# Optimization experiments

Hardware: AMD Instinct MI355X
Metric: run time of the kernel (lower is better)

Reference implementation:

```python
import jax, jax.numpy as jnp
import numpy as np

DELTA = 0.0  # default `delta` arg of forward


def _features(voxels, clust_ids, num_clusters):
    # voxels: [N,3] float, clust_ids: [N] int in [0, C)
    n = voxels.shape[0]
    seg = lambda x: jax.ops.segment_sum(x, clust_ids, num_segments=num_clusters)
    counts = seg(jnp.ones((n,), voxels.dtype))                     # [C] cluster sizes
    safe_cnt = jnp.maximum(counts, 1.0)
    center = seg(voxels) / safe_cnt[:, None]                       # [C,3] per-cluster mean
    xc = voxels - center[clust_ids]                                # [N,3] centered voxels
    cov = seg(xc[:, :, None] * xc[:, None, :])                     # [C,3,3] = x^T x per cluster
    w, v = jnp.linalg.eigh(cov)                                    # eigvals ascending (== torch.eig + argsort)
    w2 = w[:, 2]
    dirwt = jnp.where(w2 == 0, 0.0, 1.0 - w[:, 1] / jnp.where(w2 == 0, 1.0, w2))
    wd = w + DELTA
    denom = jnp.where(wd[:, 2] == 0, 1.0, wd[:, 2])
    wn = wd / denom[:, None]                                       # w normalized by largest
    eye = jnp.eye(3, dtype=voxels.dtype)
    B = (1.0 - DELTA) * jnp.einsum('cij,cj,ckj->cik', v, wn, v) + DELTA * eye  # [C,3,3]
    v0 = v[:, :, 2]                                                # [C,3] principal axis
    x0 = jnp.sum(xc * v0[clust_ids], axis=-1)                      # [N] projection on v0
    xp0 = xc - x0[:, None] * v0[clust_ids]                         # [N,3] residual
    np0 = jnp.linalg.norm(xp0, axis=1)                             # [N]
    sc = seg(x0 * np0)                                             # [C] sign score
    v0 = jnp.where((sc < 0)[:, None], -v0, v0) * dirwt[:, None]
    # len(c) < 2 branch: center = the voxel itself (mean handles it), B = delta*I, v0 = 0
    small = counts < 2.0
    B = jnp.where(small[:, None, None], DELTA * eye, B)
    v0 = jnp.where(small[:, None], 0.0, v0)
    return jnp.concatenate([center, B.reshape(num_clusters, 9), v0, counts[:, None]], axis=1)  # [C,16]


def setup_inputs() -> dict:
    key = jax.random.key(0)
    k1, k2 = jax.random.split(key)
    n, c = 4000000, 4096
    data = jax.random.normal(k1, (n, 5), dtype=jnp.float32)
    clust_ids = jax.random.randint(k2, (n,), 0, c)
    return {"data": data, "clust_ids": clust_ids, "num_clusters": c}


def reference(data, clust_ids, num_clusters):
    voxels = data[:, :3].astype(jnp.float32)
    return _features(voxels, clust_ids, num_clusters)
```

## Files before the change

kernel.cpp:

```cpp
#include <hip/hip_runtime.h>
#include <math.h>

#define NC 4096
#define OVCAP 131072
#define CAP1 8520

__device__ __forceinline__ int xcd_id() {
    return (int)__builtin_amdgcn_s_getreg(20 | (0 << 6) | ((4 - 1) << 11));
}

__device__ __forceinline__ void solve_cluster(const float mom[10], float* o,
                                              float4* pcv, float4* pvv) {
    float cntf = mom[0];
    double dn  = (double)cntf;
    double inv = 1.0 / fmax(dn, 1.0);
    double cx = mom[1] * inv, cy = mom[2] * inv, cz = mom[3] * inv;

    double a00 = (double)mom[4] - dn * cx * cx;
    double a01 = (double)mom[5] - dn * cx * cy;
    double a02 = (double)mom[6] - dn * cx * cz;
    double a11 = (double)mom[7] - dn * cy * cy;
    double a12 = (double)mom[8] - dn * cy * cz;
    double a22 = (double)mom[9] - dn * cz * cz;

    double q  = (a00 + a11 + a22) / 3.0;
    double p1 = a01 * a01 + a02 * a02 + a12 * a12;
    double b00 = a00 - q, b11 = a11 - q, b22 = a22 - q;
    double p2 = b00 * b00 + b11 * b11 + b22 * b22 + 2.0 * p1;
    double w0, w1, w2;
    if (!(p2 > 0.0)) {
        w0 = w1 = w2 = q;
    } else {
        double p  = sqrt(p2 / 6.0);
        double ip = 1.0 / p;
        double c00 = b00 * ip, c01 = a01 * ip, c02 = a02 * ip;
        double c11 = b11 * ip, c12 = a12 * ip, c22 = b22 * ip;
        double detB = c00 * (c11 * c22 - c12 * c12)
                    - c01 * (c01 * c22 - c12 * c02)
                    + c02 * (c01 * c12 - c11 * c02);
        double r = fmin(1.0, fmax(-1.0, detB * 0.5));
        double phi = acos(r) / 3.0;
        w2 = q + 2.0 * p * cos(phi);
        w0 = q + 2.0 * p * cos(phi + 2.0943951023931953);
        w1 = 3.0 * q - w2 - w0;
    }

    double denom = (w2 == 0.0) ? 1.0 : w2;
    double dirwt = (w2 == 0.0) ? 0.0 : (1.0 - w1 / w2);

    double C00 = a00 - w1, C11 = a11 - w1, C22 = a22 - w1;
    double D00 = a00 - w0, D11 = a11 - w0, D22 = a22 - w0;
    double M00 = C00 * D00 + a01 * a01 + a02 * a02;
    double M10 = a01 * D00 + C11 * a01 + a12 * a02;
    double M20 = a02 * D00 + a12 * a01 + C22 * a02;
    double M01 = C00 * a01 + a01 * D11 + a02 * a12;
    double M11 = a01 * a01 + C11 * D11 + a12 * a12;
    double M21 = a02 * a01 + a12 * D11 + C22 * a12;
    double M02 = C00 * a02 + a01 * a12 + a02 * D22;
    double M12 = a01 * a02 + C11 * a12 + a12 * D22;
    double M22 = a02 * a02 + a12 * a12 + C22 * D22;
    double n0 = M00 * M00 + M10 * M10 + M20 * M20;
    double n1 = M01 * M01 + M11 * M11 + M21 * M21;
    double n2 = M02 * M02 + M12 * M12 + M22 * M22;
    double vx, vy, vz, nn;
    if (n0 >= n1 && n0 >= n2) { vx = M00; vy = M10; vz = M20; nn = n0; }
    else if (n1 >= n2)        { vx = M01; vy = M11; vz = M21; nn = n1; }
    else                      { vx = M02; vy = M12; vz = M22; nn = n2; }
    if (nn > 1e-300) {
        double rn = 1.0 / sqrt(nn);
        vx *= rn; vy *= rn; vz *= rn;
    } else {
        vx = vy = vz = 0.0;
    }

    bool small = cntf < 2.0f;
    float bscale = small ? 0.0f : (float)(1.0 / denom);

    o[0]  = (float)cx;
    o[1]  = (float)cy;
    o[2]  = (float)cz;
    o[3]  = (float)a00 * bscale;
    o[4]  = (float)a01 * bscale;
    o[5]  = (float)a02 * bscale;
    o[6]  = (float)a01 * bscale;
    o[7]  = (float)a11 * bscale;
    o[8]  = (float)a12 * bscale;
    o[9]  = (float)a02 * bscale;
    o[10] = (float)a12 * bscale;
    o[11] = (float)a22 * bscale;
    o[15] = cntf;

    *pcv = make_float4((float)cx, (float)cy, (float)cz, (float)dirwt);
    *pvv = make_float4((float)vx, (float)vy, (float)vz, cntf);
}

__device__ __forceinline__ void ov_spill(float4 d, int id, float4* ov, int* novf,
                                         float* gmom) {
    int ovi = atomicAdd(novf, 1);
    if (ovi < OVCAP) ov[ovi] = d;
    atomicAdd(&gmom[0 * NC + id], 1.0f);
    atomicAdd(&gmom[1 * NC + id], d.x);
    atomicAdd(&gmom[2 * NC + id], d.y);
    atomicAdd(&gmom[3 * NC + id], d.z);
    atomicAdd(&gmom[4 * NC + id], d.x * d.x);
    atomicAdd(&gmom[5 * NC + id], d.x * d.y);
    atomicAdd(&gmom[6 * NC + id], d.x * d.z);
    atomicAdd(&gmom[7 * NC + id], d.y * d.y);
    atomicAdd(&gmom[8 * NC + id], d.y * d.z);
    atomicAdd(&gmom[9 * NC + id], d.z * d.z);
}

__global__ __launch_bounds__(256) void k_p1(const float* __restrict__ data,
                                            const int* __restrict__ ids,
                                            float4* __restrict__ P1,
                                            int* __restrict__ cnt1,
                                            float4* __restrict__ ov,
                                            int* __restrict__ novf,
                                            float* __restrict__ gmom, int n) {
    __shared__ float4 srt[2048];
    __shared__ int h64[64], boff[64], bglob[64];
    int tid = threadIdx.x, lane = tid & 63;
    int xcd = xcd_id() & 7;
    int ntiles = (n + 2047) >> 11;
    for (int t = blockIdx.x; t < ntiles; t += gridDim.x) {
        int vbase = t << 11;
        if (tid < 64) h64[tid] = 0;
        __syncthreads();
        float vx[8], vy[8], vz[8];
        int vid[8], vrk[8];
#pragma unroll
        for (int s = 0; s < 8; s++) {
            int v = vbase + (s << 8) + tid;
            if (v < n) {
                vx[s] = data[v * 5 + 0];
                vy[s] = data[v * 5 + 1];
                vz[s] = data[v * 5 + 2];
                int id = ids[v];
                vid[s] = id;
                vrk[s] = atomicAdd(&h64[id >> 6], 1);
            } else vid[s] = -1;
        }
        __syncthreads();
        if (tid < 64) {
            int c0 = h64[tid], sc = c0;
            for (int off = 1; off < 64; off <<= 1) {
                int u = __shfl_up(sc, off);
                if (lane >= off) sc += u;
            }
            boff[tid] = sc - c0;
            bglob[tid] = atomicAdd(&cnt1[((tid << 3) + xcd) << 4], c0);
        }
        __syncthreads();
#pragma unroll
        for (int s = 0; s < 8; s++)
            if (vid[s] >= 0)
                srt[boff[vid[s] >> 6] + vrk[s]] =
                    make_float4(vx[s], vy[s], vz[s], __int_as_float(vid[s]));
        __syncthreads();
        int tot = n - vbase;
        tot = tot > 2048 ? 2048 : tot;
        for (int i = tid; i < tot; i += 256) {
            float4 d = srt[i];
            int id = __float_as_int(d.w);
            int b = id >> 6;
            int ofs = bglob[b] + (i - boff[b]);
            if (ofs < CAP1)
                P1[(size_t)((b << 3) + xcd) * CAP1 + ofs] = d;
            else
                ov_spill(d, id, ov, novf, gmom);
        }
        __syncthreads();
    }
}

__global__ __launch_bounds__(256) void k_mom(const float4* __restrict__ P1,
                                             const int* __restrict__ cnt1,
                                             float* __restrict__ gmom) {
    __shared__ float4 srt[2048];
    __shared__ int h64[64], boff[64];
    int tid = threadIdx.x, lane = tid & 63, w4 = tid >> 6;
    int xcd = blockIdx.x & 7;
    int rest = blockIdx.x >> 3;
    int bucket = rest & 63;
    int q = rest >> 6;
    int sub = (bucket << 3) + xcd;

    int m1c = cnt1[sub << 4];
    m1c = m1c > CAP1 ? CAP1 : m1c;
    int start = (int)(((long long)m1c * q) >> 1);
    int end   = (int)(((long long)m1c * (q + 1)) >> 1);
    size_t sbase = (size_t)sub * CAP1;

    float creg = 0.0f;
    float m1 = 0, m2 = 0, m3 = 0, m4 = 0, m5 = 0, m6 = 0, m7 = 0, m8 = 0, m9 = 0;

    for (int tb = start; tb < end; tb += 2048) {
        if (tid < 64) h64[tid] = 0;
        __syncthreads();
        float4 vd[8];
        int vcid[8], vrk[8];
#pragma unroll
        for (int s = 0; s < 8; s++) {
            int i = tb + (s << 8) + tid;
            if (i < end) {
                float4 d = P1[sbase + i];
                int cid = __float_as_int(d.w) & 63;
                vd[s] = d; vcid[s] = cid;
                vrk[s] = atomicAdd(&h64[cid], 1);
            } else vcid[s] = -1;
        }
        __syncthreads();
        if (tid < 64) {
            int c0 = h64[tid], sc = c0;
            for (int off = 1; off < 64; off <<= 1) {
                int u = __shfl_up(sc, off);
                if (lane >= off) sc += u;
            }
            boff[tid] = sc - c0;
        }
        __syncthreads();
#pragma unroll
        for (int s = 0; s < 8; s++)
            if (vcid[s] >= 0) srt[boff[vcid[s]] + vrk[s]] = vd[s];
        __syncthreads();
        int len = h64[lane];
        int bo  = boff[lane];
        if (w4 == 0) creg += (float)len;
        for (int j = w4; j < len; j += 4) {
            float4 d = srt[bo + j];
            m1 += d.x; m2 += d.y; m3 += d.z;
            m4 += d.x * d.x; m5 += d.x * d.y; m6 += d.x * d.z;
            m7 += d.y * d.y; m8 += d.y * d.z; m9 += d.z * d.z;
        }
        __syncthreads();
    }

    float* comb = (float*)srt;
    float regs[10] = {creg, m1, m2, m3, m4, m5, m6, m7, m8, m9};
#pragma unroll
    for (int k = 0; k < 10; k++)
        comb[((k << 6) + lane) * 4 + w4] = regs[k];
    __syncthreads();
    for (int i = tid; i < 640; i += 256) {
        int k = i >> 6, c = i & 63;
        float* p = comb + ((k << 6) + c) * 4;
        float v = p[0] + p[1] + p[2] + p[3];
        if (v != 0.0f) atomicAdd(&gmom[k * NC + (bucket << 6) + c], v);
    }
}

__global__ __launch_bounds__(256) void k_sc(const float4* __restrict__ P1,
                                            const int* __restrict__ cnt1,
                                            const float4* __restrict__ pc,
                                            const float4* __restrict__ pv,
                                            const float4* __restrict__ ov,
                                            const int* __restrict__ novf,
                                            float* __restrict__ gsc) {
    __shared__ float4 srt[2048];
    __shared__ int h64[64], boff[64];
    int tid = threadIdx.x, lane = tid & 63, w4 = tid >> 6;
    int xcd = blockIdx.x & 7;
    int rest = blockIdx.x >> 3;
    int bucket = rest & 63;
    int q = rest >> 6;
    int sub = (bucket << 3) + xcd;

    float4 c4 = pc[(bucket << 6) + lane];
    float4 v4 = pv[(bucket << 6) + lane];

    int m1c = cnt1[sub << 4];
    m1c = m1c > CAP1 ? CAP1 : m1c;
    int start = (int)(((long long)m1c * q) >> 1);
    int end   = (int)(((long long)m1c * (q + 1)) >> 1);
    size_t sbase = (size_t)sub * CAP1;

    float screg = 0.0f;

    for (int tb = start; tb < end; tb += 2048) {
        if (tid < 64) h64[tid] = 0;
        __syncthreads();
        float4 vd[8];
        int vcid[8], vrk[8];
#pragma unroll
        for (int s = 0; s < 8; s++) {
            int i = tb + (s << 8) + tid;
            if (i < end) {
                float4 d = P1[sbase + i];
                int cid = __float_as_int(d.w) & 63;
                vd[s] = d; vcid[s] = cid;
                vrk[s] = atomicAdd(&h64[cid], 1);
            } else vcid[s] = -1;
        }
        __syncthreads();
        if (tid < 64) {
            int c0 = h64[tid], sc = c0;
            for (int off = 1; off < 64; off <<= 1) {
                int u = __shfl_up(sc, off);
                if (lane >= off) sc += u;
            }
            boff[tid] = sc - c0;
        }
        __syncthreads();
#pragma unroll
        for (int s = 0; s < 8; s++)
            if (vcid[s] >= 0) srt[boff[vcid[s]] + vrk[s]] = vd[s];
        __syncthreads();
        int len = h64[lane];
        int bo  = boff[lane];
        for (int j = w4; j < len; j += 4) {
            float4 d = srt[bo + j];
            float xc = d.x - c4.x, yc = d.y - c4.y, zc = d.z - c4.z;
            float x0 = xc * v4.x + yc * v4.y + zc * v4.z;
            float px = xc - x0 * v4.x;
            float py = yc - x0 * v4.y;
            float pz = zc - x0 * v4.z;
            screg += x0 * sqrtf(px * px + py * py + pz * pz);
        }
        __syncthreads();
    }

    if (xcd == 0 && q == 0) {
        int mo = *novf;
        mo = mo > OVCAP ? OVCAP : mo;
        for (int i = 0; i < mo; i++) {
            float4 d = ov[i];
            int id = __float_as_int(d.w);
            if (w4 == 0 && (id >> 6) == bucket && (id & 63) == lane) {
                float xc = d.x - c4.x, yc = d.y - c4.y, zc = d.z - c4.z;
                float x0 = xc * v4.x + yc * v4.y + zc * v4.z;
                float px = xc - x0 * v4.x;
                float py = yc - x0 * v4.y;
                float pz = zc - x0 * v4.z;
                screg += x0 * sqrtf(px * px + py * py + pz * pz);
            }
        }
    }

    float* comb = (float*)srt;
    comb[lane * 4 + w4] = screg;
    __syncthreads();
    if (tid < 64) {
        float* p = comb + tid * 4;
        float s = p[0] + p[1] + p[2] + p[3];
        if (s != 0.0f) atomicAdd(&gsc[(bucket << 6) + tid], s);
    }
}

__global__ void k_eigen_fb(const float* __restrict__ gmom, float* __restrict__ out,
                           float4* __restrict__ pc, float4* __restrict__ pv) {
    int c = blockIdx.x * blockDim.x + threadIdx.x;
    if (c >= NC) return;
    float mom[10];
#pragma unroll
    for (int k = 0; k < 10; k++) mom[k] = gmom[k * NC + c];
    solve_cluster(mom, out + c * 16, &pc[c], &pv[c]);
}

__global__ void k_final_fb(const float4* __restrict__ pc, const float4* __restrict__ pv,
                           const float* __restrict__ gsc, float* __restrict__ out) {
    int c = blockIdx.x * blockDim.x + threadIdx.x;
    if (c >= NC) return;
    float4 c4 = pc[c];
    float4 v4 = pv[c];
    float s = (gsc[c] < 0.0f) ? -c4.w : c4.w;
    if (v4.w < 2.0f) s = 0.0f;
    out[c * 16 + 12] = v4.x * s;
    out[c * 16 + 13] = v4.y * s;
    out[c * 16 + 14] = v4.z * s;
}

__global__ __launch_bounds__(1024) void k_accum_raw(const float* __restrict__ data,
                                                    const int* __restrict__ ids,
                                                    float* __restrict__ gmom, int n) {
    extern __shared__ float s[];
    for (int i = threadIdx.x; i < 10 * NC; i += blockDim.x) s[i] = 0.0f;
    __syncthreads();
    int stride = gridDim.x * blockDim.x;
    for (int i = blockIdx.x * blockDim.x + threadIdx.x; i < n; i += stride) {
        int id = ids[i];
        float x = data[i * 5 + 0], y = data[i * 5 + 1], z = data[i * 5 + 2];
        atomicAdd(&s[0 * NC + id], 1.0f);
        atomicAdd(&s[1 * NC + id], x);
        atomicAdd(&s[2 * NC + id], y);
        atomicAdd(&s[3 * NC + id], z);
        atomicAdd(&s[4 * NC + id], x * x);
        atomicAdd(&s[5 * NC + id], x * y);
        atomicAdd(&s[6 * NC + id], x * z);
        atomicAdd(&s[7 * NC + id], y * y);
        atomicAdd(&s[8 * NC + id], y * z);
        atomicAdd(&s[9 * NC + id], z * z);
    }
    __syncthreads();
    for (int i = threadIdx.x; i < 10 * NC; i += blockDim.x) {
        float v = s[i];
        if (v != 0.0f) atomicAdd(&gmom[i], v);
    }
}

__global__ __launch_bounds__(1024) void k_sc_raw(const float* __restrict__ data,
                                                 const int* __restrict__ ids,
                                                 const float4* __restrict__ pc,
                                                 const float4* __restrict__ pv,
                                                 float* __restrict__ gsc, int n) {
    extern __shared__ float4 sl4[];
    float4* spc = sl4;
    float4* spv = sl4 + NC;
    float*  ssc = (float*)(sl4 + 2 * NC);
    for (int i = threadIdx.x; i < NC; i += blockDim.x) {
        spc[i] = pc[i]; spv[i] = pv[i]; ssc[i] = 0.0f;
    }
    __syncthreads();
    int stride = gridDim.x * blockDim.x;
    for (int i = blockIdx.x * blockDim.x + threadIdx.x; i < n; i += stride) {
        int id = ids[i];
        float4 c4 = spc[id];
        float4 v4 = spv[id];
        float xc = data[i * 5 + 0] - c4.x;
        float yc = data[i * 5 + 1] - c4.y;
        float zc = data[i * 5 + 2] - c4.z;
        float x0 = xc * v4.x + yc * v4.y + zc * v4.z;
        float px = xc - x0 * v4.x;
        float py = yc - x0 * v4.y;
        float pz = zc - x0 * v4.z;
        atomicAdd(&ssc[id], x0 * sqrtf(px * px + py * py + pz * pz));
    }
    __syncthreads();
    for (int i = threadIdx.x; i < NC; i += blockDim.x) {
        float v = ssc[i];
        if (v != 0.0f) atomicAdd(&gsc[i], v);
    }
}

extern "C" void kernel_launch(void* const* d_in, const int* in_sizes, int n_in,
                              void* d_out, int out_size, void* d_ws, size_t ws_size,
                              hipStream_t stream) {
    const float* data = (const float*)d_in[0];
    const int*   ids  = (const int*)d_in[1];
    float* out = (float*)d_out;
    int n = in_sizes[1];

    char* ws = (char*)d_ws;
    float*  gmom = (float*)(ws);
    float*  gsc  = (float*)(ws + 163840);
    int*    cnt1 = (int*)(ws + 180224);
    int*    novf = (int*)(ws + 212992);
    float4* pc   = (float4*)(ws + 213056);
    float4* pv   = (float4*)(ws + 278592);
    float4* ov   = (float4*)(ws + 344128);
    const size_t FIXED = 2441280;
    const size_t P1SZ  = (size_t)512 * CAP1 * 16;

    if (ws_size >= FIXED + P1SZ) {
        float4* P1 = (float4*)(ws + FIXED);
        hipMemsetAsync(ws, 0, 213056, stream);
        hipLaunchKernelGGL(k_p1, dim3(2048), dim3(256), 0, stream,
                           data, ids, P1, cnt1, ov, novf, gmom, n);
        hipLaunchKernelGGL(k_mom, dim3(1024), dim3(256), 0, stream,
                           P1, cnt1, gmom);
        hipLaunchKernelGGL(k_eigen_fb, dim3(16), dim3(256), 0, stream,
                           gmom, out, pc, pv);
        hipLaunchKernelGGL(k_sc, dim3(1024), dim3(256), 0, stream,
                           P1, cnt1, pc, pv, ov, novf, gsc);
        hipLaunchKernelGGL(k_final_fb, dim3(16), dim3(256), 0, stream,
                           pc, pv, gsc, out);
    } else {
        hipMemsetAsync(ws, 0, 180224, stream);
        hipLaunchKernelGGL(k_accum_raw, dim3(256), dim3(1024), 10 * NC * 4, stream,
                           data, ids, gmom, n);
        hipLaunchKernelGGL(k_eigen_fb, dim3(16), dim3(256), 0, stream, gmom, out, pc, pv);
        hipLaunchKernelGGL(k_sc_raw, dim3(256), dim3(1024), 2 * NC * 16 + NC * 4, stream,
                           data, ids, pc, pv, gsc, n);
        hipLaunchKernelGGL(k_final_fb, dim3(16), dim3(256), 0, stream, pc, pv, gsc, out);
    }
}
```

Baseline: 227.7 us.

## Compute sign score directly from raw input with shared-memory atomics

Replaces the sign-score kernel that re-read the bucketed, partitioned copy (with an in-block counting sort per tile and an overflow pass) with a grid-stride kernel that reads the original data and ids. Each point gathers its cluster's center and axis and atomically adds its term into a per-block shared histogram of all clusters, which is then flushed to global memory with atomics. This drops the sorting and synchronisation overhead. In exchange it reads the strided 5-float rows (60 MB of row data plus 16 MB of ids) instead of the compact 16-byte records, does random gathers into pc/pv, and relies on contended shared-memory float atomics.

```diff
diff --git a/kernel.cpp b/kernel.cpp
--- a/kernel.cpp
+++ b/kernel.cpp
@@ -249,100 +249,33 @@
     }
 }
 
-__global__ __launch_bounds__(256) void k_sc(const float4* __restrict__ P1,
-                                            const int* __restrict__ cnt1,
-                                            const float4* __restrict__ pc,
-                                            const float4* __restrict__ pv,
-                                            const float4* __restrict__ ov,
-                                            const int* __restrict__ novf,
-                                            float* __restrict__ gsc) {
-    __shared__ float4 srt[2048];
-    __shared__ int h64[64], boff[64];
-    int tid = threadIdx.x, lane = tid & 63, w4 = tid >> 6;
-    int xcd = blockIdx.x & 7;
-    int rest = blockIdx.x >> 3;
-    int bucket = rest & 63;
-    int q = rest >> 6;
-    int sub = (bucket << 3) + xcd;
-
-    float4 c4 = pc[(bucket << 6) + lane];
-    float4 v4 = pv[(bucket << 6) + lane];
-
-    int m1c = cnt1[sub << 4];
-    m1c = m1c > CAP1 ? CAP1 : m1c;
-    int start = (int)(((long long)m1c * q) >> 1);
-    int end   = (int)(((long long)m1c * (q + 1)) >> 1);
-    size_t sbase = (size_t)sub * CAP1;
-
-    float screg = 0.0f;
-
-    for (int tb = start; tb < end; tb += 2048) {
-        if (tid < 64) h64[tid] = 0;
-        __syncthreads();
-        float4 vd[8];
-        int vcid[8], vrk[8];
-#pragma unroll
-        for (int s = 0; s < 8; s++) {
-            int i = tb + (s << 8) + tid;
-            if (i < end) {
-                float4 d = P1[sbase + i];
-                int cid = __float_as_int(d.w) & 63;
-                vd[s] = d; vcid[s] = cid;
-                vrk[s] = atomicAdd(&h64[cid], 1);
-            } else vcid[s] = -1;
-        }
-        __syncthreads();
-        if (tid < 64) {
-            int c0 = h64[tid], sc = c0;
-            for (int off = 1; off < 64; off <<= 1) {
-                int u = __shfl_up(sc, off);
-                if (lane >= off) sc += u;
-            }
-            boff[tid] = sc - c0;
-        }
-        __syncthreads();
-#pragma unroll
-        for (int s = 0; s < 8; s++)
-            if (vcid[s] >= 0) srt[boff[vcid[s]] + vrk[s]] = vd[s];
-        __syncthreads();
-        int len = h64[lane];
-        int bo  = boff[lane];
-        for (int j = w4; j < len; j += 4) {
-            float4 d = srt[bo + j];
-            float xc = d.x - c4.x, yc = d.y - c4.y, zc = d.z - c4.z;
-            float x0 = xc * v4.x + yc * v4.y + zc * v4.z;
-            float px = xc - x0 * v4.x;
-            float py = yc - x0 * v4.y;
-            float pz = zc - x0 * v4.z;
-            screg += x0 * sqrtf(px * px + py * py + pz * pz);
-        }
-        __syncthreads();
-    }
-
-    if (xcd == 0 && q == 0) {
-        int mo = *novf;
-        mo = mo > OVCAP ? OVCAP : mo;
-        for (int i = 0; i < mo; i++) {
-            float4 d = ov[i];
-            int id = __float_as_int(d.w);
-            if (w4 == 0 && (id >> 6) == bucket && (id & 63) == lane) {
-                float xc = d.x - c4.x, yc = d.y - c4.y, zc = d.z - c4.z;
-                float x0 = xc * v4.x + yc * v4.y + zc * v4.z;
-                float px = xc - x0 * v4.x;
-                float py = yc - x0 * v4.y;
-                float pz = zc - x0 * v4.z;
-                screg += x0 * sqrtf(px * px + py * py + pz * pz);
-            }
-        }
-    }
-
-    float* comb = (float*)srt;
-    comb[lane * 4 + w4] = screg;
-    __syncthreads();
-    if (tid < 64) {
-        float* p = comb + tid * 4;
-        float s = p[0] + p[1] + p[2] + p[3];
-        if (s != 0.0f) atomicAdd(&gsc[(bucket << 6) + tid], s);
+__global__ __launch_bounds__(512) void k_scd(const float* __restrict__ data,
+                                             const int* __restrict__ ids,
+                                             const float4* __restrict__ pc,
+                                             const float4* __restrict__ pv,
+                                             float* __restrict__ gsc, int n) {
+    __shared__ float ssc[NC];
+    int tid = threadIdx.x;
+    for (int i = tid; i < NC; i += 512) ssc[i] = 0.0f;
+    __syncthreads();
+    int stride = gridDim.x * 512;
+    for (int i = blockIdx.x * 512 + tid; i < n; i += stride) {
+        int id = ids[i];
+        float4 c4 = pc[id];
+        float4 v4 = pv[id];
+        float xc = data[i * 5 + 0] - c4.x;
+        float yc = data[i * 5 + 1] - c4.y;
+        float zc = data[i * 5 + 2] - c4.z;
+        float x0 = xc * v4.x + yc * v4.y + zc * v4.z;
+        float px = xc - x0 * v4.x;
+        float py = yc - x0 * v4.y;
+        float pz = zc - x0 * v4.z;
+        atomicAdd(&ssc[id], x0 * sqrtf(px * px + py * py + pz * pz));
+    }
+    __syncthreads();
+    for (int i = tid; i < NC; i += 512) {
+        float v = ssc[i];
+        if (v != 0.0f) atomicAdd(&gsc[i], v);
     }
 }
 
@@ -459,8 +392,8 @@
                            P1, cnt1, gmom);
         hipLaunchKernelGGL(k_eigen_fb, dim3(16), dim3(256), 0, stream,
                            gmom, out, pc, pv);
-        hipLaunchKernelGGL(k_sc, dim3(1024), dim3(256), 0, stream,
-                           P1, cnt1, pc, pv, ov, novf, gsc);
+        hipLaunchKernelGGL(k_scd, dim3(256), dim3(512), 0, stream,
+                           data, ids, pc, pv, gsc, n);
         hipLaunchKernelGGL(k_final_fb, dim3(16), dim3(256), 0, stream,
                            pc, pv, gsc, out);
     } else {
```

Result: slower. 236.7 us (+4.0%).
